# Optimization experiments

Measured on AMD Instinct MI355X. Metric: run time of the kernel, lower is better.

The kernel has to match this reference:

```python
import jax, jax.numpy as jnp
import numpy as np

# SLAYER SRM-alpha neuron constants (from network.yaml defaults)
THETA = 10.0      # spike threshold
TAU_S = 10.0      # PSP (srm) time constant
TAU_R = 1.0       # refractory time constant
TS = 1.0          # simulation timestep
TAU_RHO = 1.0     # surrogate gradient width
SCALE_RHO = 1.0   # surrogate gradient scale
E = float(np.e)

@jax.custom_vjp
def spike_fn(v):
    # Heaviside threshold; surrogate gradient in bwd (SLAYER spike pdf)
    return (v >= 0).astype(v.dtype)

def _spike_fwd(v):
    return spike_fn(v), v

def _spike_bwd(v, g):
    sg = (SCALE_RHO / TAU_RHO) * jnp.exp(-jnp.abs(v) / TAU_RHO)
    return (g * sg,)

spike_fn.defvjp(_spike_fwd, _spike_bwd)

def psp_spike(a):
    """SLAYER psp (alpha SRM kernel eps(t)=(t/tau_s)e^{1-t/tau_s}, IIR form)
    followed by spike generation with refractory feedback
    nu(t) = -2*theta*(t/tau_r)e^{1-t/tau_r}. a: [B,C,T] -> spikes [B,C,T].
    Alpha kernels realized exactly as 2-state linear recursions."""
    ds = jnp.exp(jnp.asarray(-TS / TAU_S, a.dtype))
    dr = jnp.exp(jnp.asarray(-TS / TAU_R, a.dtype))
    cs = E / TAU_S
    cr = -2.0 * THETA * E / TAU_R
    B, C, T = a.shape
    z = jnp.zeros((B, C), a.dtype)

    def step(carry, a_t):
        xs, ys, xr, yr = carry
        u = cs * ys + cr * yr          # membrane = psp(a) + refractory
        s = spike_fn(u - THETA)
        xs = ds * xs + a_t             # first-order stage (input)
        ys = ds * (ys + TS * xs)       # alpha stage: ys[t+1]=d*(ys+Ts*xs)
        xr = dr * xr + s               # refractory stages driven by spikes
        yr = dr * (yr + TS * xr)
        return (xs, ys, xr, yr), s

    _, s = jax.lax.scan(step, (z, z, z, z), jnp.moveaxis(a, -1, 0))
    return jnp.moveaxis(s, 0, -1)

def psp(a):
    """Pure SLAYER psp filter (no spiking). a: [B,C,T] -> [B,C,T]."""
    ds = jnp.exp(jnp.asarray(-TS / TAU_S, a.dtype))
    cs = E / TAU_S
    B, C, T = a.shape
    z = jnp.zeros((B, C), a.dtype)

    def step(carry, a_t):
        xs, ys = carry
        p = cs * ys
        xs = ds * xs + a_t
        ys = ds * (ys + TS * xs)
        return (xs, ys), p

    _, p = jax.lax.scan(step, (z, z), jnp.moveaxis(a, -1, 0))
    return jnp.moveaxis(p, 0, -1)

def setup_inputs() -> dict:
    key = jax.random.key(0)
    k1, k2, k3 = jax.random.split(key, 3)
    B, NIN, H, NOUT, T = 64, 4, 512, 2, 2000
    # sparse binary input spike trains, rate ~0.1
    spikeInput = (jax.random.uniform(k1, (B, NIN, T)) < 0.1).astype(jnp.float32)
    W1 = 2.0 * jax.random.normal(k2, (H, NIN), jnp.float32)
    W2 = 2.0 * jax.random.normal(k3, (NOUT, H), jnp.float32)
    return {"spikeInput": spikeInput, "W1": W1, "W2": W2}

def reference(spikeInput, W1, W2):
    # fc1 -> psp -> spike
    s1 = psp_spike(jnp.einsum('oi,bit->bot', W1, spikeInput))
    # fc2 -> psp -> spike
    s2 = psp_spike(jnp.einsum('oh,bht->bot', W2, s1))
    # final psp readout
    return psp(s2)
```

## Files before the change

### kernel.cpp

```cpp
#include <hip/hip_runtime.h>
#include <cstdint>
#include <cstddef>

#define THETA_F 10.0f
#define DS_C 0.9048374180359595731642491f
#define DR_C 0.3678794411714423215955238f
#define CS_C 0.2718281828459045235360287f
#define CR_C -54.3656365691809047072057f
#define P40_C 1.8315638888734179e-02f
#define Q40_C 6.6290701607045023e-01f

typedef unsigned int       u32;
typedef unsigned long long u64;
typedef unsigned short     u16;

#define W32_WORDS_PER_B  (62 * 512)
#define TAIL_BYTE_OFF    (64 * 62 * 512 * 4)

__global__ __launch_bounds__(128) void k1_layer1(
    const float* __restrict__ inp,
    const float* __restrict__ W1,
    u32* __restrict__ w32, u16* __restrict__ tail16)
{
    __shared__ float table[16 * 128];
    __shared__ alignas(8) unsigned char codes[2048];

    const int tid = threadIdx.x;
    const int b   = blockIdx.x >> 2;
    const int h   = ((blockIdx.x & 3) << 7) + tid;

    const float w0 = W1[h * 4 + 0];
    const float w1 = W1[h * 4 + 1];
    const float w2 = W1[h * 4 + 2];
    const float w3 = W1[h * 4 + 3];
    for (int c = 0; c < 16; ++c) {
        float v = __fmul_rn(w0, (c & 1) ? 1.0f : 0.0f);
        v = __fadd_rn(v, __fmul_rn(w1, (c & 2) ? 1.0f : 0.0f));
        v = __fadd_rn(v, __fmul_rn(w2, (c & 4) ? 1.0f : 0.0f));
        v = __fadd_rn(v, __fmul_rn(w3, (c & 8) ? 1.0f : 0.0f));
        table[c * 128 + tid] = v;
    }
    for (int t = tid; t < 2000; t += 128) {
        const float v0 = inp[(b * 4 + 0) * 2000 + t];
        const float v1 = inp[(b * 4 + 1) * 2000 + t];
        const float v2 = inp[(b * 4 + 2) * 2000 + t];
        const float v3 = inp[(b * 4 + 3) * 2000 + t];
        codes[t] = (unsigned char)((int)(v0 != 0.0f) | ((int)(v1 != 0.0f) << 1) |
                                   ((int)(v2 != 0.0f) << 2) | ((int)(v3 != 0.0f) << 3));
    }
    if (tid < 48) codes[2000 + tid] = 0;
    __syncthreads();

#define ISSUE(CW, BUF) do {                                                   \
        const u32 lo_ = (u32)(CW), hi_ = (u32)((CW) >> 32);                   \
        BUF[0] = table[((lo_      ) & 15) * 128 + tid];                       \
        BUF[1] = table[((lo_ >>  8) & 15) * 128 + tid];                       \
        BUF[2] = table[((lo_ >> 16) & 15) * 128 + tid];                       \
        BUF[3] = table[((lo_ >> 24) & 15) * 128 + tid];                       \
        BUF[4] = table[((hi_      ) & 15) * 128 + tid];                       \
        BUF[5] = table[((hi_ >>  8) & 15) * 128 + tid];                       \
        BUF[6] = table[((hi_ >> 16) & 15) * 128 + tid];                       \
        BUF[7] = table[((hi_ >> 24) & 15) * 128 + tid];                       \
    } while (0)

#define STEP(AV, BITPOS) do {                                                 \
        const float u_ = __fadd_rn(__fmul_rn(CS_C, ys), __fmul_rn(CR_C, yr)); \
        const bool sp_ = (u_ >= THETA_F);                                     \
        xs = __fadd_rn(__fmul_rn(DS_C, xs), (AV));                            \
        ys = __fmul_rn(DS_C, __fadd_rn(ys, xs));                              \
        const float A_ = __fmul_rn(DR_C, xr);                                 \
        xr = sp_ ? __fadd_rn(A_, 1.0f) : A_;                                  \
        yr = __fmul_rn(DR_C, __fadd_rn(yr, xr));                              \
        bits = sp_ ? (bits | (1u << (BITPOS))) : bits;                        \
    } while (0)

#define STEP8(BUF, J0) do {                                                   \
        _Pragma("unroll")                                                     \
        for (int j_ = 0; j_ < 8; ++j_) STEP(BUF[j_], (J0) + j_);              \
    } while (0)

    float xs = 0.0f, ys = 0.0f, xr = 0.0f, yr = 0.0f;
    u32 bits = 0;
    u32* pw = w32 + (size_t)b * W32_WORDS_PER_B + h;

    float bA[8], bB[8];
    u64 cw = *reinterpret_cast<const u64*>(codes);
    ISSUE(cw, bA);
    u64 c1 = *reinterpret_cast<const u64*>(codes + 8);
    u64 c2 = *reinterpret_cast<const u64*>(codes + 16);
    u64 c3 = *reinterpret_cast<const u64*>(codes + 24);
    u64 c4 = *reinterpret_cast<const u64*>(codes + 32);

    for (int t0 = 0; t0 < 1984; t0 += 32) {
        ISSUE(c1, bB);
        const u64 n1 = *reinterpret_cast<const u64*>(codes + t0 + 40);
        const u64 n2 = *reinterpret_cast<const u64*>(codes + t0 + 48);
        const u64 n3 = *reinterpret_cast<const u64*>(codes + t0 + 56);
        const u64 n4 = *reinterpret_cast<const u64*>(codes + t0 + 64);
        STEP8(bA, 0);
        ISSUE(c2, bA);
        STEP8(bB, 8);
        ISSUE(c3, bB);
        STEP8(bA, 16);
        ISSUE(c4, bA);
        STEP8(bB, 24);
        *pw = bits; pw += 512; bits = 0;
        c1 = n1; c2 = n2; c3 = n3; c4 = n4;
    }
    ISSUE(c1, bB);
    STEP8(bA, 0);
    STEP8(bB, 8);
    tail16[b * 512 + h] = (u16)bits;

#undef STEP8
#undef STEP
#undef ISSUE
}

__global__ __launch_bounds__(256) void k2_fc2(
    const u32* __restrict__ w32, const u16* __restrict__ tail16,
    const float* __restrict__ W2,
    float* __restrict__ a2)
{
    __shared__ float w2s[1024];
    __shared__ u32 stage[4096];

    const int tid = threadIdx.x;
    const int b  = blockIdx.x >> 3;
    const int it = blockIdx.x & 7;

    for (int j = tid; j < 1024; j += 256) w2s[j] = W2[j];
    #pragma unroll
    for (int k = 0; k < 16; ++k) {
        const int l = tid + (k << 8);
        const int gtb = (it << 3) + (l >> 9);
        u32 v = 0;
        if (gtb < 62)       v = w32[((size_t)b * 62 + gtb) * 512 + (l & 511)];
        else if (gtb == 62) v = (u32)tail16[b * 512 + (l & 511)];
        stage[l] = v;
    }
    __syncthreads();

    const int t = (it << 8) + tid;
    if (t < 2000) {
        const u32* srow = stage + ((tid >> 5) << 9);
        const int sh = tid & 31;
        float acc0 = 0.0f, acc1 = 0.0f;
        #pragma unroll 8
        for (int hh = 0; hh < 512; ++hh) {
            const bool on = (srow[hh] >> sh) & 1u;
            acc0 = __fadd_rn(acc0, on ? w2s[hh] : 0.0f);
            acc1 = __fadd_rn(acc1, on ? w2s[512 + hh] : 0.0f);
        }
        a2[(size_t)(b * 2 + 0) * 2000 + t] = acc0;
        a2[(size_t)(b * 2 + 1) * 2000 + t] = acc1;
    }
}

__global__ __launch_bounds__(200) void k3all(
    const float* __restrict__ a2, float* __restrict__ out)
{
    __shared__ float U[4][2000];
    __shared__ unsigned char s2b[4][2000];
    __shared__ float ex[4][50], ey[4][50], px[4][50], py[4][50];

    const int tid = threadIdx.x;
    const int lc  = tid / 50;
    const int ck  = tid - lc * 50;
    const int chain = blockIdx.x * 4 + lc;

    {
        const float* segi = a2 + (size_t)chain * 2000 + ck * 40;
        float* segU = &U[lc][ck * 40];
        float X = 0.0f, Y = 0.0f;
        for (int g = 0; g < 10; ++g) {
            float4 qv = *reinterpret_cast<const float4*>(segi + 4 * g);
            float z;
            z = __fmul_rn(CS_C, Y); X = __fmaf_rn(DS_C, X, qv.x);
            Y = __fmul_rn(DS_C, __fadd_rn(Y, X)); qv.x = z;
            z = __fmul_rn(CS_C, Y); X = __fmaf_rn(DS_C, X, qv.y);
            Y = __fmul_rn(DS_C, __fadd_rn(Y, X)); qv.y = z;
            z = __fmul_rn(CS_C, Y); X = __fmaf_rn(DS_C, X, qv.z);
            Y = __fmul_rn(DS_C, __fadd_rn(Y, X)); qv.z = z;
            z = __fmul_rn(CS_C, Y); X = __fmaf_rn(DS_C, X, qv.w);
            Y = __fmul_rn(DS_C, __fadd_rn(Y, X)); qv.w = z;
            *reinterpret_cast<float4*>(segU + 4 * g) = qv;
        }
        ex[lc][ck] = X; ey[lc][ck] = Y;
    }
    __syncthreads();
    if (tid < 4) {
        float x = 0.0f, y = 0.0f;
        for (int c = 0; c < 50; ++c) {
            px[tid][c] = x; py[tid][c] = y;
            const float xn = __fmaf_rn(P40_C, x, ex[tid][c]);
            const float yn = __fadd_rn(
                __fmaf_rn(Q40_C, x, __fmul_rn(P40_C, y)), ey[tid][c]);
            x = xn; y = yn;
        }
    }
    __syncthreads();
    {
        float xh = px[lc][ck], yh = py[lc][ck];
        float* segU = &U[lc][ck * 40];
        if (ck != 0) {
            for (int g = 0; g < 10; ++g) {
                float4 qv = *reinterpret_cast<const float4*>(segU + 4 * g);
                qv.x = __fmaf_rn(CS_C, yh, qv.x);
                xh = __fmul_rn(DS_C, xh); yh = __fmul_rn(DS_C, __fadd_rn(yh, xh));
                qv.y = __fmaf_rn(CS_C, yh, qv.y);
                xh = __fmul_rn(DS_C, xh); yh = __fmul_rn(DS_C, __fadd_rn(yh, xh));
                qv.z = __fmaf_rn(CS_C, yh, qv.z);
                xh = __fmul_rn(DS_C, xh); yh = __fmul_rn(DS_C, __fadd_rn(yh, xh));
                qv.w = __fmaf_rn(CS_C, yh, qv.w);
                xh = __fmul_rn(DS_C, xh); yh = __fmul_rn(DS_C, __fadd_rn(yh, xh));
                *reinterpret_cast<float4*>(segU + 4 * g) = qv;
            }
        }
    }
    __syncthreads();

    {
        float xr2 = 0.0f, yr2 = 0.0f;
#define RSTEP(UV) do {                                                        \
        const float u_ = __fadd_rn((UV), __fmul_rn(CR_C, yr2));               \
        const bool sp_ = (u_ >= THETA_F);                                     \
        const float A_ = __fmul_rn(DR_C, xr2);                                \
        xr2 = sp_ ? __fadd_rn(A_, 1.0f) : A_;                                 \
        yr2 = __fmul_rn(DR_C, __fadd_rn(yr2, xr2));                           \
    } while (0)
        if (ck == 1) {
            const float* wseg = &U[lc][0];
            #pragma unroll
            for (int g = 0; g < 10; ++g) {
                const float4 qv = *reinterpret_cast<const float4*>(wseg + 4 * g);
                RSTEP(qv.x); RSTEP(qv.y); RSTEP(qv.z); RSTEP(qv.w);
            }
        } else if (ck >= 2) {
            const float* wseg = &U[lc][ck * 40 - 64];
            #pragma unroll
            for (int g = 0; g < 16; ++g) {
                const float4 qv = *reinterpret_cast<const float4*>(wseg + 4 * g);
                RSTEP(qv.x); RSTEP(qv.y); RSTEP(qv.z); RSTEP(qv.w);
            }
        }
        const float* eseg = &U[lc][ck * 40];
        unsigned char* ob = &s2b[lc][ck * 40];
        for (int g = 0; g < 10; ++g) {
            const float4 qv = *reinterpret_cast<const float4*>(eseg + 4 * g);
            const float uv[4] = {qv.x, qv.y, qv.z, qv.w};
            #pragma unroll
            for (int j = 0; j < 4; ++j) {
                const float u_ = __fadd_rn(uv[j], __fmul_rn(CR_C, yr2));
                const bool sp_ = (u_ >= THETA_F);
                ob[4 * g + j] = sp_ ? 1 : 0;
                const float A_ = __fmul_rn(DR_C, xr2);
                xr2 = sp_ ? __fadd_rn(A_, 1.0f) : A_;
                yr2 = __fmul_rn(DR_C, __fadd_rn(yr2, xr2));
            }
        }
#undef RSTEP
    }
    __syncthreads();

    float* sego = out + (size_t)chain * 2000 + ck * 40;
    {
        const unsigned char* si = &s2b[lc][ck * 40];
        float X = 0.0f, Y = 0.0f;
        for (int j = 0; j < 40; ++j) {
            const float a = (float)si[j];
            const float z = __fmul_rn(CS_C, Y);
            X = __fmaf_rn(DS_C, X, a);
            Y = __fmul_rn(DS_C, __fadd_rn(Y, X));
            sego[j] = z;
        }
        ex[lc][ck] = X; ey[lc][ck] = Y;
    }
    __syncthreads();
    if (tid < 4) {
        float x = 0.0f, y = 0.0f;
        for (int c = 0; c < 50; ++c) {
            px[tid][c] = x; py[tid][c] = y;
            const float xn = __fmaf_rn(P40_C, x, ex[tid][c]);
            const float yn = __fadd_rn(
                __fmaf_rn(Q40_C, x, __fmul_rn(P40_C, y)), ey[tid][c]);
            x = xn; y = yn;
        }
    }
    __syncthreads();
    {
        float xh = px[lc][ck], yh = py[lc][ck];
        if (ck != 0) {
            for (int j = 0; j < 40; ++j) {
                sego[j] = __fmaf_rn(CS_C, yh, sego[j]);
                xh = __fmul_rn(DS_C, xh);
                yh = __fmul_rn(DS_C, __fadd_rn(yh, xh));
            }
        }
    }
}

extern "C" void kernel_launch(void* const* d_in, const int* in_sizes, int n_in,
                              void* d_out, int out_size, void* d_ws, size_t ws_size,
                              hipStream_t stream)
{
    const float* inp = (const float*)d_in[0];
    const float* W1  = (const float*)d_in[1];
    const float* W2  = (const float*)d_in[2];
    float* out = (float*)d_out;

    u32* w32    = (u32*)d_ws;
    u16* tail16 = (u16*)((char*)d_ws + TAIL_BYTE_OFF);

    k1_layer1<<<dim3(256), dim3(128), 0, stream>>>(inp, W1, w32, tail16);
    k2_fc2<<<dim3(512), dim3(256), 0, stream>>>(w32, tail16, W2, out);
    k3all<<<dim3(32), dim3(200), 0, stream>>>(out, out);
}
```

Measured before the change: 137.6 us.

## Fuse three layer kernels into one cooperative kernel with grid syncs

Merges the layer-1 spiking kernel, the fc2 reduction and the final layer-2/readout kernel into a single cooperative launch of 256 blocks, with grid-wide syncs between stages and a shared memory buffer reused across them. This removes two kernel launch gaps and the tail/drain between dependent launches. It also changes the work split: fc2 now runs on 256 blocks of 128 threads instead of 512 blocks of 256, and the final stage uses one chain per block over 128 blocks instead of four chains per block over 32. The cost is grid-sync overhead, 128 of the 256 blocks sitting idle in the last stage, and fewer threads for the fc2 stage.

```diff
diff --git a/kernel.cpp b/kernel.cpp
--- a/kernel.cpp
+++ b/kernel.cpp
@@ -1,6 +1,9 @@
 #include <hip/hip_runtime.h>
+#include <hip/hip_cooperative_groups.h>
 #include <cstdint>
 #include <cstddef>
+
+namespace cg = cooperative_groups;
 
 #define THETA_F 10.0f
 #define DS_C 0.9048374180359595731642491f
@@ -17,39 +20,47 @@
 #define W32_WORDS_PER_B  (62 * 512)
 #define TAIL_BYTE_OFF    (64 * 62 * 512 * 4)
 
-__global__ __launch_bounds__(128) void k1_layer1(
+__global__ __launch_bounds__(128) void fused_all(
     const float* __restrict__ inp,
     const float* __restrict__ W1,
-    u32* __restrict__ w32, u16* __restrict__ tail16)
+    const float* __restrict__ W2,
+    u32* __restrict__ w32, u16* __restrict__ tail16,
+    float* __restrict__ out)
 {
-    __shared__ float table[16 * 128];
-    __shared__ alignas(8) unsigned char codes[2048];
+    __shared__ alignas(16) char smem[38912];
 
     const int tid = threadIdx.x;
-    const int b   = blockIdx.x >> 2;
-    const int h   = ((blockIdx.x & 3) << 7) + tid;
-
-    const float w0 = W1[h * 4 + 0];
-    const float w1 = W1[h * 4 + 1];
-    const float w2 = W1[h * 4 + 2];
-    const float w3 = W1[h * 4 + 3];
-    for (int c = 0; c < 16; ++c) {
-        float v = __fmul_rn(w0, (c & 1) ? 1.0f : 0.0f);
-        v = __fadd_rn(v, __fmul_rn(w1, (c & 2) ? 1.0f : 0.0f));
-        v = __fadd_rn(v, __fmul_rn(w2, (c & 4) ? 1.0f : 0.0f));
-        v = __fadd_rn(v, __fmul_rn(w3, (c & 8) ? 1.0f : 0.0f));
-        table[c * 128 + tid] = v;
-    }
-    for (int t = tid; t < 2000; t += 128) {
-        const float v0 = inp[(b * 4 + 0) * 2000 + t];
-        const float v1 = inp[(b * 4 + 1) * 2000 + t];
-        const float v2 = inp[(b * 4 + 2) * 2000 + t];
-        const float v3 = inp[(b * 4 + 3) * 2000 + t];
-        codes[t] = (unsigned char)((int)(v0 != 0.0f) | ((int)(v1 != 0.0f) << 1) |
-                                   ((int)(v2 != 0.0f) << 2) | ((int)(v3 != 0.0f) << 3));
-    }
-    if (tid < 48) codes[2000 + tid] = 0;
-    __syncthreads();
+    const int blk = blockIdx.x;
+    const int b   = blk >> 2;
+    const int q   = blk & 3;
+
+    {
+        float* table = (float*)smem;
+        unsigned char* codes = (unsigned char*)(smem + 8192);
+
+        const int h = (q << 7) + tid;
+
+        const float w0 = W1[h * 4 + 0];
+        const float w1 = W1[h * 4 + 1];
+        const float w2 = W1[h * 4 + 2];
+        const float w3 = W1[h * 4 + 3];
+        for (int c = 0; c < 16; ++c) {
+            float v = __fmul_rn(w0, (c & 1) ? 1.0f : 0.0f);
+            v = __fadd_rn(v, __fmul_rn(w1, (c & 2) ? 1.0f : 0.0f));
+            v = __fadd_rn(v, __fmul_rn(w2, (c & 4) ? 1.0f : 0.0f));
+            v = __fadd_rn(v, __fmul_rn(w3, (c & 8) ? 1.0f : 0.0f));
+            table[c * 128 + tid] = v;
+        }
+        for (int t = tid; t < 2000; t += 128) {
+            const float v0 = inp[(b * 4 + 0) * 2000 + t];
+            const float v1 = inp[(b * 4 + 1) * 2000 + t];
+            const float v2 = inp[(b * 4 + 2) * 2000 + t];
+            const float v3 = inp[(b * 4 + 3) * 2000 + t];
+            codes[t] = (unsigned char)((int)(v0 != 0.0f) | ((int)(v1 != 0.0f) << 1) |
+                                       ((int)(v2 != 0.0f) << 2) | ((int)(v3 != 0.0f) << 3));
+        }
+        if (tid < 48) codes[2000 + tid] = 0;
+        __syncthreads();
 
 #define ISSUE(CW, BUF) do {                                                   \
         const u32 lo_ = (u32)(CW), hi_ = (u32)((CW) >> 32);                   \
@@ -79,131 +90,134 @@
         for (int j_ = 0; j_ < 8; ++j_) STEP(BUF[j_], (J0) + j_);              \
     } while (0)
 
-    float xs = 0.0f, ys = 0.0f, xr = 0.0f, yr = 0.0f;
-    u32 bits = 0;
-    u32* pw = w32 + (size_t)b * W32_WORDS_PER_B + h;
-
-    float bA[8], bB[8];
-    u64 cw = *reinterpret_cast<const u64*>(codes);
-    ISSUE(cw, bA);
-    u64 c1 = *reinterpret_cast<const u64*>(codes + 8);
-    u64 c2 = *reinterpret_cast<const u64*>(codes + 16);
-    u64 c3 = *reinterpret_cast<const u64*>(codes + 24);
-    u64 c4 = *reinterpret_cast<const u64*>(codes + 32);
-
-    for (int t0 = 0; t0 < 1984; t0 += 32) {
+        float xs = 0.0f, ys = 0.0f, xr = 0.0f, yr = 0.0f;
+        u32 bits = 0;
+        u32* pw = w32 + (size_t)b * W32_WORDS_PER_B + h;
+
+        float bA[8], bB[8];
+        u64 cw = *reinterpret_cast<const u64*>(codes);
+        ISSUE(cw, bA);
+        u64 c1 = *reinterpret_cast<const u64*>(codes + 8);
+        u64 c2 = *reinterpret_cast<const u64*>(codes + 16);
+        u64 c3 = *reinterpret_cast<const u64*>(codes + 24);
+        u64 c4 = *reinterpret_cast<const u64*>(codes + 32);
+
+        for (int t0 = 0; t0 < 1984; t0 += 32) {
+            ISSUE(c1, bB);
+            const u64 n1 = *reinterpret_cast<const u64*>(codes + t0 + 40);
+            const u64 n2 = *reinterpret_cast<const u64*>(codes + t0 + 48);
+            const u64 n3 = *reinterpret_cast<const u64*>(codes + t0 + 56);
+            const u64 n4 = *reinterpret_cast<const u64*>(codes + t0 + 64);
+            STEP8(bA, 0);
+            ISSUE(c2, bA);
+            STEP8(bB, 8);
+            ISSUE(c3, bB);
+            STEP8(bA, 16);
+            ISSUE(c4, bA);
+            STEP8(bB, 24);
+            *pw = bits; pw += 512; bits = 0;
+            c1 = n1; c2 = n2; c3 = n3; c4 = n4;
+        }
         ISSUE(c1, bB);
-        const u64 n1 = *reinterpret_cast<const u64*>(codes + t0 + 40);
-        const u64 n2 = *reinterpret_cast<const u64*>(codes + t0 + 48);
-        const u64 n3 = *reinterpret_cast<const u64*>(codes + t0 + 56);
-        const u64 n4 = *reinterpret_cast<const u64*>(codes + t0 + 64);
         STEP8(bA, 0);
-        ISSUE(c2, bA);
         STEP8(bB, 8);
-        ISSUE(c3, bB);
-        STEP8(bA, 16);
-        ISSUE(c4, bA);
-        STEP8(bB, 24);
-        *pw = bits; pw += 512; bits = 0;
-        c1 = n1; c2 = n2; c3 = n3; c4 = n4;
-    }
-    ISSUE(c1, bB);
-    STEP8(bA, 0);
-    STEP8(bB, 8);
-    tail16[b * 512 + h] = (u16)bits;
+        tail16[b * 512 + h] = (u16)bits;
 
 #undef STEP8
 #undef STEP
 #undef ISSUE
-}
-
-__global__ __launch_bounds__(256) void k2_fc2(
-    const u32* __restrict__ w32, const u16* __restrict__ tail16,
-    const float* __restrict__ W2,
-    float* __restrict__ a2)
-{
-    __shared__ float w2s[1024];
-    __shared__ u32 stage[4096];
-
-    const int tid = threadIdx.x;
-    const int b  = blockIdx.x >> 3;
-    const int it = blockIdx.x & 7;
-
-    for (int j = tid; j < 1024; j += 256) w2s[j] = W2[j];
-    #pragma unroll
-    for (int k = 0; k < 16; ++k) {
-        const int l = tid + (k << 8);
-        const int gtb = (it << 3) + (l >> 9);
-        u32 v = 0;
-        if (gtb < 62)       v = w32[((size_t)b * 62 + gtb) * 512 + (l & 511)];
-        else if (gtb == 62) v = (u32)tail16[b * 512 + (l & 511)];
-        stage[l] = v;
     }
-    __syncthreads();
-
-    const int t = (it << 8) + tid;
-    if (t < 2000) {
-        const u32* srow = stage + ((tid >> 5) << 9);
-        const int sh = tid & 31;
-        float acc0 = 0.0f, acc1 = 0.0f;
-        #pragma unroll 8
-        for (int hh = 0; hh < 512; ++hh) {
-            const bool on = (srow[hh] >> sh) & 1u;
-            acc0 = __fadd_rn(acc0, on ? w2s[hh] : 0.0f);
-            acc1 = __fadd_rn(acc1, on ? w2s[512 + hh] : 0.0f);
-        }
-        a2[(size_t)(b * 2 + 0) * 2000 + t] = acc0;
-        a2[(size_t)(b * 2 + 1) * 2000 + t] = acc1;
+
+    cg::this_grid().sync();
+
+    {
+        u32* stage = (u32*)smem;
+        float* w2s = (float*)(smem + 34816);
+
+        const int t_lo  = q * 500;
+        const int tb_lo = t_lo >> 5;
+        const int tb_hi = (t_lo + 499) >> 5;
+        const int nst   = (tb_hi - tb_lo + 1) << 9;
+
+        for (int idx = tid; idx < nst; idx += 128) {
+            const int gtb = tb_lo + (idx >> 9);
+            const int hh  = idx & 511;
+            u32 v = 0;
+            if (gtb < 62)       v = w32[((size_t)b * 62 + gtb) * 512 + hh];
+            else if (gtb == 62) v = (u32)tail16[b * 512 + hh];
+            stage[idx] = v;
+        }
+        for (int j = tid; j < 1024; j += 128) w2s[j] = W2[j];
+        __syncthreads();
+
+        for (int k = 0; k < 4; ++k) {
+            const int off = (k << 7) + tid;
+            if (off < 500) {
+                const int t   = t_lo + off;
+                const u32* srow = stage + (((t >> 5) - tb_lo) << 9);
+                const int sh  = t & 31;
+                float acc0 = 0.0f, acc1 = 0.0f;
+                #pragma unroll 8
+                for (int hh = 0; hh < 512; ++hh) {
+                    const bool on = (srow[hh] >> sh) & 1u;
+                    acc0 = __fadd_rn(acc0, on ? w2s[hh] : 0.0f);
+                    acc1 = __fadd_rn(acc1, on ? w2s[512 + hh] : 0.0f);
+                }
+                out[(size_t)(b * 2 + 0) * 2000 + t] = acc0;
+                out[(size_t)(b * 2 + 1) * 2000 + t] = acc1;
+            }
+        }
+        __syncthreads();
     }
-}
-
-__global__ __launch_bounds__(200) void k3all(
-    const float* __restrict__ a2, float* __restrict__ out)
-{
-    __shared__ float U[4][2000];
-    __shared__ unsigned char s2b[4][2000];
-    __shared__ float ex[4][50], ey[4][50], px[4][50], py[4][50];
-
-    const int tid = threadIdx.x;
-    const int lc  = tid / 50;
-    const int ck  = tid - lc * 50;
-    const int chain = blockIdx.x * 4 + lc;
+
+    cg::this_grid().sync();
 
     {
-        const float* segi = a2 + (size_t)chain * 2000 + ck * 40;
-        float* segU = &U[lc][ck * 40];
-        float X = 0.0f, Y = 0.0f;
-        for (int g = 0; g < 10; ++g) {
-            float4 qv = *reinterpret_cast<const float4*>(segi + 4 * g);
-            float z;
-            z = __fmul_rn(CS_C, Y); X = __fmaf_rn(DS_C, X, qv.x);
-            Y = __fmul_rn(DS_C, __fadd_rn(Y, X)); qv.x = z;
-            z = __fmul_rn(CS_C, Y); X = __fmaf_rn(DS_C, X, qv.y);
-            Y = __fmul_rn(DS_C, __fadd_rn(Y, X)); qv.y = z;
-            z = __fmul_rn(CS_C, Y); X = __fmaf_rn(DS_C, X, qv.z);
-            Y = __fmul_rn(DS_C, __fadd_rn(Y, X)); qv.z = z;
-            z = __fmul_rn(CS_C, Y); X = __fmaf_rn(DS_C, X, qv.w);
-            Y = __fmul_rn(DS_C, __fadd_rn(Y, X)); qv.w = z;
-            *reinterpret_cast<float4*>(segU + 4 * g) = qv;
-        }
-        ex[lc][ck] = X; ey[lc][ck] = Y;
-    }
-    __syncthreads();
-    if (tid < 4) {
-        float x = 0.0f, y = 0.0f;
-        for (int c = 0; c < 50; ++c) {
-            px[tid][c] = x; py[tid][c] = y;
-            const float xn = __fmaf_rn(P40_C, x, ex[tid][c]);
-            const float yn = __fadd_rn(
-                __fmaf_rn(Q40_C, x, __fmul_rn(P40_C, y)), ey[tid][c]);
-            x = xn; y = yn;
-        }
-    }
-    __syncthreads();
-    {
-        float xh = px[lc][ck], yh = py[lc][ck];
-        float* segU = &U[lc][ck * 40];
-        if (ck != 0) {
+        float* U            = (float*)smem;
+        unsigned char* s2b  = (unsigned char*)(smem + 8000);
+        float* ex = (float*)(smem + 10000);
+        float* ey = (float*)(smem + 10208);
+        float* px = (float*)(smem + 10416);
+        float* py = (float*)(smem + 10624);
+
+        const bool p3 = (blk < 128);
+        const int chain = blk;
+        const int ck = tid;
+
+        if (p3 && ck < 50) {
+            const float* segi = out + (size_t)chain * 2000 + ck * 40;
+            float* segU = &U[ck * 40];
+            float X = 0.0f, Y = 0.0f;
+            for (int g = 0; g < 10; ++g) {
+                float4 qv = *reinterpret_cast<const float4*>(segi + 4 * g);
+                float z;
+                z = __fmul_rn(CS_C, Y); X = __fmaf_rn(DS_C, X, qv.x);
+                Y = __fmul_rn(DS_C, __fadd_rn(Y, X)); qv.x = z;
+                z = __fmul_rn(CS_C, Y); X = __fmaf_rn(DS_C, X, qv.y);
+                Y = __fmul_rn(DS_C, __fadd_rn(Y, X)); qv.y = z;
+                z = __fmul_rn(CS_C, Y); X = __fmaf_rn(DS_C, X, qv.z);
+                Y = __fmul_rn(DS_C, __fadd_rn(Y, X)); qv.z = z;
+                z = __fmul_rn(CS_C, Y); X = __fmaf_rn(DS_C, X, qv.w);
+                Y = __fmul_rn(DS_C, __fadd_rn(Y, X)); qv.w = z;
+                *reinterpret_cast<float4*>(segU + 4 * g) = qv;
+            }
+            ex[ck] = X; ey[ck] = Y;
+        }
+        __syncthreads();
+        if (p3 && tid == 0) {
+            float x = 0.0f, y = 0.0f;
+            for (int c = 0; c < 50; ++c) {
+                px[c] = x; py[c] = y;
+                const float xn = __fmaf_rn(P40_C, x, ex[c]);
+                const float yn = __fadd_rn(
+                    __fmaf_rn(Q40_C, x, __fmul_rn(P40_C, y)), ey[c]);
+                x = xn; y = yn;
+            }
+        }
+        __syncthreads();
+        if (p3 && ck >= 1 && ck < 50) {
+            float xh = px[ck], yh = py[ck];
+            float* segU = &U[ck * 40];
             for (int g = 0; g < 10; ++g) {
                 float4 qv = *reinterpret_cast<const float4*>(segU + 4 * g);
                 qv.x = __fmaf_rn(CS_C, yh, qv.x);
@@ -217,11 +231,10 @@
                 *reinterpret_cast<float4*>(segU + 4 * g) = qv;
             }
         }
-    }
-    __syncthreads();
-
-    {
-        float xr2 = 0.0f, yr2 = 0.0f;
+        __syncthreads();
+
+        if (p3 && ck < 50) {
+            float xr2 = 0.0f, yr2 = 0.0f;
 #define RSTEP(UV) do {                                                        \
         const float u_ = __fadd_rn((UV), __fmul_rn(CR_C, yr2));               \
         const bool sp_ = (u_ >= THETA_F);                                     \
@@ -229,68 +242,68 @@
         xr2 = sp_ ? __fadd_rn(A_, 1.0f) : A_;                                 \
         yr2 = __fmul_rn(DR_C, __fadd_rn(yr2, xr2));                           \
     } while (0)
-        if (ck == 1) {
-            const float* wseg = &U[lc][0];
-            #pragma unroll
+            if (ck == 1) {
+                const float* wseg = &U[0];
+                #pragma unroll
+                for (int g = 0; g < 10; ++g) {
+                    const float4 qv = *reinterpret_cast<const float4*>(wseg + 4 * g);
+                    RSTEP(qv.x); RSTEP(qv.y); RSTEP(qv.z); RSTEP(qv.w);
+                }
+            } else if (ck >= 2) {
+                const float* wseg = &U[ck * 40 - 64];
+                #pragma unroll
+                for (int g = 0; g < 16; ++g) {
+                    const float4 qv = *reinterpret_cast<const float4*>(wseg + 4 * g);
+                    RSTEP(qv.x); RSTEP(qv.y); RSTEP(qv.z); RSTEP(qv.w);
+                }
+            }
+            const float* eseg = &U[ck * 40];
+            unsigned char* ob = &s2b[ck * 40];
             for (int g = 0; g < 10; ++g) {
-                const float4 qv = *reinterpret_cast<const float4*>(wseg + 4 * g);
-                RSTEP(qv.x); RSTEP(qv.y); RSTEP(qv.z); RSTEP(qv.w);
-            }
-        } else if (ck >= 2) {
-            const float* wseg = &U[lc][ck * 40 - 64];
-            #pragma unroll
-            for (int g = 0; g < 16; ++g) {
-                const float4 qv = *reinterpret_cast<const float4*>(wseg + 4 * g);
-                RSTEP(qv.x); RSTEP(qv.y); RSTEP(qv.z); RSTEP(qv.w);
-            }
-        }
-        const float* eseg = &U[lc][ck * 40];
-        unsigned char* ob = &s2b[lc][ck * 40];
-        for (int g = 0; g < 10; ++g) {
-            const float4 qv = *reinterpret_cast<const float4*>(eseg + 4 * g);
-            const float uv[4] = {qv.x, qv.y, qv.z, qv.w};
-            #pragma unroll
-            for (int j = 0; j < 4; ++j) {
-                const float u_ = __fadd_rn(uv[j], __fmul_rn(CR_C, yr2));
-                const bool sp_ = (u_ >= THETA_F);
-                ob[4 * g + j] = sp_ ? 1 : 0;
-                const float A_ = __fmul_rn(DR_C, xr2);
-                xr2 = sp_ ? __fadd_rn(A_, 1.0f) : A_;
-                yr2 = __fmul_rn(DR_C, __fadd_rn(yr2, xr2));
-            }
-        }
+                const float4 qv = *reinterpret_cast<const float4*>(eseg + 4 * g);
+                const float uv[4] = {qv.x, qv.y, qv.z, qv.w};
+                #pragma unroll
+                for (int j = 0; j < 4; ++j) {
+                    const float u_ = __fadd_rn(uv[j], __fmul_rn(CR_C, yr2));
+                    const bool sp_ = (u_ >= THETA_F);
+                    ob[4 * g + j] = sp_ ? 1 : 0;
+                    const float A_ = __fmul_rn(DR_C, xr2);
+                    xr2 = sp_ ? __fadd_rn(A_, 1.0f) : A_;
+                    yr2 = __fmul_rn(DR_C, __fadd_rn(yr2, xr2));
+                }
+            }
 #undef RSTEP
-    }
-    __syncthreads();
-
-    float* sego = out + (size_t)chain * 2000 + ck * 40;
-    {
-        const unsigned char* si = &s2b[lc][ck * 40];
-        float X = 0.0f, Y = 0.0f;
-        for (int j = 0; j < 40; ++j) {
-            const float a = (float)si[j];
-            const float z = __fmul_rn(CS_C, Y);
-            X = __fmaf_rn(DS_C, X, a);
-            Y = __fmul_rn(DS_C, __fadd_rn(Y, X));
-            sego[j] = z;
-        }
-        ex[lc][ck] = X; ey[lc][ck] = Y;
-    }
-    __syncthreads();
-    if (tid < 4) {
-        float x = 0.0f, y = 0.0f;
-        for (int c = 0; c < 50; ++c) {
-            px[tid][c] = x; py[tid][c] = y;
-            const float xn = __fmaf_rn(P40_C, x, ex[tid][c]);
-            const float yn = __fadd_rn(
-                __fmaf_rn(Q40_C, x, __fmul_rn(P40_C, y)), ey[tid][c]);
-            x = xn; y = yn;
-        }
-    }
-    __syncthreads();
-    {
-        float xh = px[lc][ck], yh = py[lc][ck];
-        if (ck != 0) {
+        }
+        __syncthreads();
+
+        if (p3 && ck < 50) {
+            float* sego = out + (size_t)chain * 2000 + ck * 40;
+            const unsigned char* si = &s2b[ck * 40];
+            float X = 0.0f, Y = 0.0f;
+            for (int j = 0; j < 40; ++j) {
+                const float a = (float)si[j];
+                const float z = __fmul_rn(CS_C, Y);
+                X = __fmaf_rn(DS_C, X, a);
+                Y = __fmul_rn(DS_C, __fadd_rn(Y, X));
+                sego[j] = z;
+            }
+            ex[ck] = X; ey[ck] = Y;
+        }
+        __syncthreads();
+        if (p3 && tid == 0) {
+            float x = 0.0f, y = 0.0f;
+            for (int c = 0; c < 50; ++c) {
+                px[c] = x; py[c] = y;
+                const float xn = __fmaf_rn(P40_C, x, ex[c]);
+                const float yn = __fadd_rn(
+                    __fmaf_rn(Q40_C, x, __fmul_rn(P40_C, y)), ey[c]);
+                x = xn; y = yn;
+            }
+        }
+        __syncthreads();
+        if (p3 && ck >= 1 && ck < 50) {
+            float* sego = out + (size_t)chain * 2000 + ck * 40;
+            float xh = px[ck], yh = py[ck];
             for (int j = 0; j < 40; ++j) {
                 sego[j] = __fmaf_rn(CS_C, yh, sego[j]);
                 xh = __fmul_rn(DS_C, xh);
@@ -312,7 +325,8 @@
     u32* w32    = (u32*)d_ws;
     u16* tail16 = (u16*)((char*)d_ws + TAIL_BYTE_OFF);
 
-    k1_layer1<<<dim3(256), dim3(128), 0, stream>>>(inp, W1, w32, tail16);
-    k2_fc2<<<dim3(512), dim3(256), 0, stream>>>(w32, tail16, W2, out);
-    k3all<<<dim3(32), dim3(200), 0, stream>>>(out, out);
+    void* args[] = { (void*)&inp, (void*)&W1, (void*)&W2,
+                     (void*)&w32, (void*)&tail16, (void*)&out };
+    hipLaunchCooperativeKernel((const void*)fused_all, dim3(256), dim3(128),
+                               args, 0, stream);
 }
```

New measurement: 292.4 us. 113% more time.
